# Kernel tuning notes

Hardware: AMD Instinct MI355X
Metric: run time of the kernel (lower is better)

Reference implementation:

```python
import jax, jax.numpy as jnp
import numpy as np

B, T, I, H, L, O = 512, 512, 64, 256, 3, 1  # batch, seq_len, input, hidden, layers, output


def setup_inputs() -> dict:
    key = jax.random.key(0)
    ks = jax.random.split(key, 16)
    s = 1.0 / np.sqrt(H)  # PyTorch nn.RNN init: U(-1/sqrt(H), 1/sqrt(H))
    u = lambda k, shape: jax.random.uniform(k, shape, jnp.float32, -s, s)
    inp = {"x": jax.random.normal(ks[0], (B, T, I), jnp.float32)}
    in_sizes = [I, H, H]
    for l in range(L):
        inp[f"w_ih{l}"] = u(ks[1 + 4 * l], (H, in_sizes[l]))
        inp[f"w_hh{l}"] = u(ks[2 + 4 * l], (H, H))
        inp[f"b_ih{l}"] = u(ks[3 + 4 * l], (H,))
        inp[f"b_hh{l}"] = u(ks[4 + 4 * l], (H,))
    inp["w_fc"] = u(ks[13], (O, H))
    inp["b_fc"] = u(ks[14], (O,))
    return inp


def _rnn_layer(x, w_ih, w_hh, b_ih, b_hh):
    # x: [B, T, in] -> outputs [B, T, H]; h_t = tanh(x_t W_ih^T + b_ih + h_{t-1} W_hh^T + b_hh)
    pre = jnp.einsum('bti,hi->bth', x, w_ih) + b_ih + b_hh  # input projection for all t at once

    def step(h, p_t):
        h = jnp.tanh(p_t + h @ w_hh.T)
        return h, h

    h0 = jnp.zeros((x.shape[0], w_hh.shape[0]), x.dtype)
    _, ys = jax.lax.scan(step, h0, pre.transpose(1, 0, 2))  # scan over time
    return ys.transpose(1, 0, 2)


def reference(x, w_ih0, w_hh0, b_ih0, b_hh0, w_ih1, w_hh1, b_ih1, b_hh1,
              w_ih2, w_hh2, b_ih2, b_hh2, w_fc, b_fc):
    h = _rnn_layer(x, w_ih0, w_hh0, b_ih0, b_hh0)
    h = _rnn_layer(h, w_ih1, w_hh1, b_ih1, b_hh1)
    h = _rnn_layer(h, w_ih2, w_hh2, b_ih2, b_hh2)
    out = h[:, -1, :] @ w_fc.T + b_fc  # [B, 1]
    return out.squeeze()  # [B]
```

## Files before the change

### kernel.cpp

```cpp
#include <hip/hip_runtime.h>
#include <cstdint>
#include <cstddef>

#define Tsz 512
#define TC  32
#define NCH 16

typedef _Float16 f16;
typedef _Float16 half8_t __attribute__((ext_vector_type(8)));
typedef _Float16 half4_t __attribute__((ext_vector_type(4)));
typedef float float4_t __attribute__((ext_vector_type(4)));

__device__ __forceinline__ float fast_exp2(float x) {
  float r; asm("v_exp_f32 %0, %1" : "=v"(r) : "v"(x)); return r;
}
__device__ __forceinline__ void pin(half8_t& v) { asm("" : "+v"(v)); }

#define BARRIER_LG asm volatile("s_waitcnt lgkmcnt(0)\n\ts_barrier" ::: "memory")

__device__ __forceinline__ size_t poff(int tile, int slot, int t, int j, int q) {
  return (((size_t)((tile * 2 + slot) * TC + t) * 256 + j) << 6) + ((size_t)q << 4);
}

template<int LAYER>
__device__ __forceinline__ void rec01_body(
    char* const smem, const int chunk, const int tile,
    const float* __restrict__ Pin, float* __restrict__ Pout,
    const f16* __restrict__ whh_h, const f16* __restrict__ wihn_h,
    const float* __restrict__ biasc, f16* __restrict__ st)
{
  char* const h_lds = smem;
  const int tid  = threadIdx.x;
  const int lane = tid & 63;
  const int wave = tid >> 6;
  const int m    = lane & 15;
  const int q    = lane >> 4;
  const int lo   = m * 16;
  const int slot = chunk & 1;

  half8_t whh[2][8], wihn[2][8];
  float biasn[2];
#pragma unroll
  for (int jt = 0; jt < 2; ++jt) {
    const int j = wave * 32 + jt * 16 + m;
    biasn[jt] = biasc[(LAYER + 1) * 256 + j];
#pragma unroll
    for (int c = 0; c < 8; ++c) whh[jt][c]  = *(const half8_t*)(whh_h  + j * 256 + c * 32 + q * 8);
#pragma unroll
    for (int c = 0; c < 8; ++c) wihn[jt][c] = *(const half8_t*)(wihn_h + j * 256 + c * 32 + q * 8);
  }
#pragma unroll
  for (int jt = 0; jt < 2; ++jt) {
#pragma unroll
    for (int c = 0; c < 8; ++c) { pin(whh[jt][c]); pin(wihn[jt][c]); }
  }

  if (chunk == 0)
    *(float4_t*)(h_lds + tid * 16) = float4_t{0.f, 0.f, 0.f, 0.f};
  else
    *(float4_t*)(h_lds + tid * 16) = *(const float4_t*)((const char*)st + tile * 8192 + tid * 16);

  float4_t pld[2][2];
  auto pload = [&](int tl, float4_t* d) {
    const int tn = (tl > TC - 1) ? (TC - 1) : tl;
    const char* gb = (const char*)Pin + poff(tile, slot, tn, wave * 32 + m, q);
    d[0] = *(const float4_t*)gb;
    d[1] = *(const float4_t*)(gb + 1024);
  };
  pload(0, pld[0]); pload(1, pld[1]);
  BARRIER_LG;

#pragma unroll 4
  for (int tl = 0; tl < TC; ++tl) {
    char* cur = h_lds + (tl & 1) * 8192;
    char* nxt = h_lds + ((tl + 1) & 1) * 8192;

    half8_t hf[8];
#pragma unroll
    for (int c = 0; c < 8; ++c) hf[c] = *(const half8_t*)(cur + (c * 4 + q) * 256 + lo);

    float4_t acc[2];
#pragma unroll
    for (int jt = 0; jt < 2; ++jt) {
      float4_t a = pld[tl & 1][jt];
#pragma unroll
      for (int c = 0; c < 8; ++c)
        a = __builtin_amdgcn_mfma_f32_16x16x32_f16(hf[c], whh[jt][c], a, 0, 0, 0);
      acc[jt] = a;
    }
    pload(tl + 2, pld[tl & 1]);

    if (tl >= 1) {
#pragma unroll
      for (int jt = 0; jt < 2; ++jt) {
        float4_t b = {biasn[jt], biasn[jt], biasn[jt], biasn[jt]};
#pragma unroll
        for (int c = 0; c < 8; ++c)
          b = __builtin_amdgcn_mfma_f32_16x16x32_f16(hf[c], wihn[jt][c], b, 0, 0, 0);
        *(float4_t*)((char*)Pout + poff(tile, slot, tl - 1, wave * 32 + jt * 16 + m, q)) = b;
      }
    }

#pragma unroll
    for (int jt = 0; jt < 2; ++jt) {
      const int j = wave * 32 + jt * 16 + m;
#pragma unroll
      for (int r = 0; r < 4; ++r) {
        const float e  = fast_exp2(acc[jt][r] * 2.8853900817779268f);
        const float hv = 1.0f - 2.0f * __builtin_amdgcn_rcpf(1.0f + e);
        const int b = q * 4 + r;
        *(f16*)(nxt + (j >> 3) * 256 + b * 16 + (j & 7) * 2) = (f16)hv;
      }
    }
    BARRIER_LG;
  }

  {
    half8_t hf[8];
#pragma unroll
    for (int c = 0; c < 8; ++c) hf[c] = *(const half8_t*)(h_lds + (c * 4 + q) * 256 + lo);
#pragma unroll
    for (int jt = 0; jt < 2; ++jt) {
      float4_t b = {biasn[jt], biasn[jt], biasn[jt], biasn[jt]};
#pragma unroll
      for (int c = 0; c < 8; ++c)
        b = __builtin_amdgcn_mfma_f32_16x16x32_f16(hf[c], wihn[jt][c], b, 0, 0, 0);
      *(float4_t*)((char*)Pout + poff(tile, slot, TC - 1, wave * 32 + jt * 16 + m, q)) = b;
    }
  }
  *(float4_t*)((char*)st + tile * 8192 + tid * 16) = *(const float4_t*)(h_lds + tid * 16);
}

template<bool REC, bool PRE>
__device__ __forceinline__ void l2_body(
    char* const smem, const int chunk, const int pre_chunk, const int tile,
    const float* __restrict__ x, const float* __restrict__ Pin, float* __restrict__ Pout,
    const f16* __restrict__ whh_h, const f16* __restrict__ wih0_h,
    const float* __restrict__ biasc, f16* __restrict__ st)
{
  char* const h_lds = smem;
  const int tid  = threadIdx.x;
  const int lane = tid & 63;
  const int wave = tid >> 6;
  const int m    = lane & 15;
  const int q    = lane >> 4;
  const int lo   = m * 16;
  const int slot  = chunk & 1;
  const int pslot = pre_chunk & 1;

  half8_t whh[2][8], wih0[2][2];
  float bias0[2];
#pragma unroll
  for (int jt = 0; jt < 2; ++jt) {
    const int j = wave * 32 + jt * 16 + m;
    if constexpr (PRE) {
      bias0[jt] = biasc[j];
#pragma unroll
      for (int c = 0; c < 2; ++c) wih0[jt][c] = *(const half8_t*)(wih0_h + j * 64 + c * 32 + q * 8);
    }
    if constexpr (REC) {
#pragma unroll
      for (int c = 0; c < 8; ++c) whh[jt][c] = *(const half8_t*)(whh_h + j * 256 + c * 32 + q * 8);
    }
  }
#pragma unroll
  for (int jt = 0; jt < 2; ++jt) {
    if constexpr (REC) {
#pragma unroll
      for (int c = 0; c < 8; ++c) pin(whh[jt][c]);
    }
    if constexpr (PRE) { pin(wih0[jt][0]); pin(wih0[jt][1]); }
  }

  float4_t pld[2][2];
  auto pload = [&](int tl, float4_t* d) {
    const int tn = (tl > TC - 1) ? (TC - 1) : tl;
    const char* gb = (const char*)Pin + poff(tile, slot, tn, wave * 32 + m, q);
    d[0] = *(const float4_t*)gb;
    d[1] = *(const float4_t*)(gb + 1024);
  };
  float4_t xp[2][4];
  auto xload = [&](int tl, float4_t* d) {
    const int tn = (tl > TC - 1) ? (TC - 1) : tl;
    const float* base = x + ((size_t)(tile * 16 + m) * Tsz + (pre_chunk * TC + tn)) * 64 + q * 8;
    d[0] = *(const float4_t*)base;        d[1] = *(const float4_t*)(base + 4);
    d[2] = *(const float4_t*)(base + 32); d[3] = *(const float4_t*)(base + 36);
  };

  if constexpr (REC) {
    if (chunk == 0)
      *(float4_t*)(h_lds + tid * 16) = float4_t{0.f, 0.f, 0.f, 0.f};
    else
      *(float4_t*)(h_lds + tid * 16) = *(const float4_t*)((const char*)st + tile * 8192 + tid * 16);
    pload(0, pld[0]); pload(1, pld[1]);
  }
  if constexpr (PRE) { xload(0, xp[0]); xload(1, xp[1]); }
  if constexpr (REC) BARRIER_LG;

#pragma unroll 4
  for (int tl = 0; tl < TC; ++tl) {
    if constexpr (REC) {
      char* cur = h_lds + (tl & 1) * 8192;
      char* nxt = h_lds + ((tl + 1) & 1) * 8192;
      half8_t hf[8];
#pragma unroll
      for (int c = 0; c < 8; ++c) hf[c] = *(const half8_t*)(cur + (c * 4 + q) * 256 + lo);
      float4_t acc[2];
#pragma unroll
      for (int jt = 0; jt < 2; ++jt) {
        float4_t a = pld[tl & 1][jt];
#pragma unroll
        for (int c = 0; c < 8; ++c)
          a = __builtin_amdgcn_mfma_f32_16x16x32_f16(hf[c], whh[jt][c], a, 0, 0, 0);
        acc[jt] = a;
      }
      pload(tl + 2, pld[tl & 1]);
#pragma unroll
      for (int jt = 0; jt < 2; ++jt) {
        const int j = wave * 32 + jt * 16 + m;
#pragma unroll
        for (int r = 0; r < 4; ++r) {
          const float e  = fast_exp2(acc[jt][r] * 2.8853900817779268f);
          const float hv = 1.0f - 2.0f * __builtin_amdgcn_rcpf(1.0f + e);
          const int b = q * 4 + r;
          *(f16*)(nxt + (j >> 3) * 256 + b * 16 + (j & 7) * 2) = (f16)hv;
        }
      }
    }
    if constexpr (PRE) {
      half8_t xf[2];
      const float4_t* xr = xp[tl & 1];
#pragma unroll
      for (int c = 0; c < 2; ++c)
#pragma unroll
        for (int u = 0; u < 8; ++u) xf[c][u] = (f16)xr[c * 2 + (u >> 2)][u & 3];
      xload(tl + 2, xp[tl & 1]);
#pragma unroll
      for (int jt = 0; jt < 2; ++jt) {
        float4_t b = {bias0[jt], bias0[jt], bias0[jt], bias0[jt]};
#pragma unroll
        for (int c = 0; c < 2; ++c)
          b = __builtin_amdgcn_mfma_f32_16x16x32_f16(xf[c], wih0[jt][c], b, 0, 0, 0);
        *(float4_t*)((char*)Pout + poff(tile, pslot, tl, wave * 32 + jt * 16 + m, q)) = b;
      }
    }
    if constexpr (REC) BARRIER_LG;
  }

  if constexpr (REC)
    *(float4_t*)((char*)st + tile * 8192 + tid * 16) = *(const float4_t*)(h_lds + tid * 16);
}

__global__ __launch_bounds__(512, 1)
void rnn_chunk_kernel(const float* __restrict__ x,
                      float* P0, float* P1, float* P2,
                      const f16* __restrict__ whh0h, const f16* __restrict__ whh1h,
                      const f16* __restrict__ whh2h, const f16* __restrict__ wih0h,
                      const f16* __restrict__ wih1h, const f16* __restrict__ wih2h,
                      const float* __restrict__ biasc,
                      f16* st0, f16* st1, f16* st2, int k)
{
  __shared__ __align__(16) char smem[16384];
  const int layer = blockIdx.x >> 5;
  const int tile  = blockIdx.x & 31;
  if (layer == 0) {
    if (k < NCH) rec01_body<0>(smem, k, tile, P0, P1, whh0h, wih1h, biasc, st0);
  } else if (layer == 1) {
    const int c = k - 1;
    if (c >= 0 && c < NCH) rec01_body<1>(smem, c, tile, P1, P2, whh1h, wih2h, biasc, st1);
  } else {
    const int c  = k - 2;
    const int pc = k + 1;
    const bool rec = (c >= 0 && c < NCH);
    const bool pre = (pc < NCH);
    if (rec && pre)  l2_body<true,  true >(smem, c, pc, tile, x, P2, P0, whh2h, wih0h, biasc, st2);
    else if (rec)    l2_body<true,  false>(smem, c, pc, tile, x, P2, P0, whh2h, wih0h, biasc, st2);
    else if (pre)    l2_body<false, true >(smem, c, pc, tile, x, P2, P0, whh2h, wih0h, biasc, st2);
  }
}

__global__ __launch_bounds__(512, 1)
void pre0_kernel(const float* __restrict__ x, float* P0,
                 const f16* __restrict__ wih0h, const float* __restrict__ biasc)
{
  __shared__ __align__(16) char smem[16384];
  l2_body<false, true>(smem, 0, 0, blockIdx.x, x, nullptr, P0, nullptr, wih0h, biasc, nullptr);
}

__global__ void prep_kernel(const float* __restrict__ wih0, const float* __restrict__ whh0,
                            const float* __restrict__ bih0, const float* __restrict__ bhh0,
                            const float* __restrict__ wih1, const float* __restrict__ whh1,
                            const float* __restrict__ bih1, const float* __restrict__ bhh1,
                            const float* __restrict__ wih2, const float* __restrict__ whh2,
                            const float* __restrict__ bih2, const float* __restrict__ bhh2,
                            f16* wih0h, f16* whh0h, f16* wih1h, f16* whh1h,
                            f16* wih2h, f16* whh2h, float* biasc)
{
  const int i = blockIdx.x * 256 + threadIdx.x;
  if      (i < 16384)  wih0h[i]          = (f16)wih0[i];
  else if (i < 81920)  whh0h[i - 16384]  = (f16)whh0[i - 16384];
  else if (i < 147456) wih1h[i - 81920]  = (f16)wih1[i - 81920];
  else if (i < 212992) whh1h[i - 147456] = (f16)whh1[i - 147456];
  else if (i < 278528) wih2h[i - 212992] = (f16)wih2[i - 212992];
  else if (i < 344064) whh2h[i - 278528] = (f16)whh2[i - 278528];
  else if (i < 344320) biasc[i - 344064]       = bih0[i - 344064] + bhh0[i - 344064];
  else if (i < 344576) biasc[256 + i - 344320] = bih1[i - 344320] + bhh1[i - 344320];
  else if (i < 344832) biasc[512 + i - 344576] = bih2[i - 344576] + bhh2[i - 344576];
}

__global__ void fc_kernel(const f16* __restrict__ st2, const float* __restrict__ w_fc,
                          const float* __restrict__ b_fc, float* __restrict__ outp) {
  const int b = blockIdx.x;
  const int lane = threadIdx.x;
  const int tile = b >> 4, bl = b & 15;
  const int j = lane * 4;
  const char* hp = (const char*)st2 + tile * 8192 + (j >> 3) * 256 + bl * 16 + (j & 7) * 2;
  const half4_t hv = *(const half4_t*)hp;
  const float4_t w = *(const float4_t*)(w_fc + j);
  float s = (float)hv[0] * w[0] + (float)hv[1] * w[1] + (float)hv[2] * w[2] + (float)hv[3] * w[3];
#pragma unroll
  for (int off = 32; off > 0; off >>= 1) s += __shfl_down(s, off, 64);
  if (lane == 0) outp[b] = s + b_fc[0];
}

extern "C" void kernel_launch(void* const* d_in, const int* in_sizes, int n_in,
                              void* d_out, int out_size, void* d_ws, size_t ws_size,
                              hipStream_t stream) {
  const float* x     = (const float*)d_in[0];
  const float* w_ih0 = (const float*)d_in[1];
  const float* w_hh0 = (const float*)d_in[2];
  const float* b_ih0 = (const float*)d_in[3];
  const float* b_hh0 = (const float*)d_in[4];
  const float* w_ih1 = (const float*)d_in[5];
  const float* w_hh1 = (const float*)d_in[6];
  const float* b_ih1 = (const float*)d_in[7];
  const float* b_hh1 = (const float*)d_in[8];
  const float* w_ih2 = (const float*)d_in[9];
  const float* w_hh2 = (const float*)d_in[10];
  const float* b_ih2 = (const float*)d_in[11];
  const float* b_hh2 = (const float*)d_in[12];
  const float* w_fc  = (const float*)d_in[13];
  const float* b_fc  = (const float*)d_in[14];

  char* ws = (char*)d_ws;
  float* P0   = (float*)(ws);
  float* P1   = (float*)(ws + 33554432);
  float* P2   = (float*)(ws + 67108864);
  f16* st0    = (f16*)(ws + 100663296);
  f16* st1    = (f16*)(ws + 100925440);
  f16* st2    = (f16*)(ws + 101187584);
  f16* wih0h  = (f16*)(ws + 101449728);
  f16* whh0h  = (f16*)(ws + 101482496);
  f16* wih1h  = (f16*)(ws + 101613568);
  f16* whh1h  = (f16*)(ws + 101744640);
  f16* wih2h  = (f16*)(ws + 101875712);
  f16* whh2h  = (f16*)(ws + 102006784);
  float* biasc = (float*)(ws + 102137856);

  prep_kernel<<<1347, 256, 0, stream>>>(w_ih0, w_hh0, b_ih0, b_hh0,
                                        w_ih1, w_hh1, b_ih1, b_hh1,
                                        w_ih2, w_hh2, b_ih2, b_hh2,
                                        wih0h, whh0h, wih1h, whh1h, wih2h, whh2h, biasc);
  pre0_kernel<<<32, 512, 0, stream>>>(x, P0, wih0h, biasc);
  for (int k = 0; k < NCH + 2; ++k)
    rnn_chunk_kernel<<<96, 512, 0, stream>>>(x, P0, P1, P2,
                                             whh0h, whh1h, whh2h,
                                             wih0h, wih1h, wih2h,
                                             biasc, st0, st1, st2, k);
  fc_kernel<<<512, 64, 0, stream>>>(st2, w_fc, b_fc, (float*)d_out);
}
```

Baseline: 1.033 ms.

## Halve waves per block, give each wave 64 hidden units, split MFMA accumulator chains

Each block now runs 4 waves of 256 threads instead of 8, so each wave owns 64 hidden columns (4 j-tiles) and holds twice as many weight registers. The MFMA reduction over K is split into two independent accumulator chains that are summed at the end, which shortens the serial dependency. The next-layer input projection is moved after the per-step barrier so it can overlap with other waves' work, and the barrier placement in the layer-2 body changes to match. Fewer waves means cheaper barriers but more register pressure and more serial MFMA work per wave on the recurrence critical path.

New measurement: 1.154 ms. 1.12x slower.

```diff
diff --git a/kernel.cpp b/kernel.cpp
--- a/kernel.cpp
+++ b/kernel.cpp
@@ -38,11 +38,11 @@
   const int lo   = m * 16;
   const int slot = chunk & 1;
 
-  half8_t whh[2][8], wihn[2][8];
-  float biasn[2];
-#pragma unroll
-  for (int jt = 0; jt < 2; ++jt) {
-    const int j = wave * 32 + jt * 16 + m;
+  half8_t whh[4][8], wihn[4][8];
+  float biasn[4];
+#pragma unroll
+  for (int jt = 0; jt < 4; ++jt) {
+    const int j = wave * 64 + jt * 16 + m;
     biasn[jt] = biasc[(LAYER + 1) * 256 + j];
 #pragma unroll
     for (int c = 0; c < 8; ++c) whh[jt][c]  = *(const half8_t*)(whh_h  + j * 256 + c * 32 + q * 8);
@@ -50,27 +50,30 @@
     for (int c = 0; c < 8; ++c) wihn[jt][c] = *(const half8_t*)(wihn_h + j * 256 + c * 32 + q * 8);
   }
 #pragma unroll
-  for (int jt = 0; jt < 2; ++jt) {
+  for (int jt = 0; jt < 4; ++jt) {
 #pragma unroll
     for (int c = 0; c < 8; ++c) { pin(whh[jt][c]); pin(wihn[jt][c]); }
   }
 
-  if (chunk == 0)
-    *(float4_t*)(h_lds + tid * 16) = float4_t{0.f, 0.f, 0.f, 0.f};
-  else
-    *(float4_t*)(h_lds + tid * 16) = *(const float4_t*)((const char*)st + tile * 8192 + tid * 16);
-
-  float4_t pld[2][2];
+  if (chunk == 0) {
+    *(float4_t*)(h_lds + tid * 32)      = float4_t{0.f, 0.f, 0.f, 0.f};
+    *(float4_t*)(h_lds + tid * 32 + 16) = float4_t{0.f, 0.f, 0.f, 0.f};
+  } else {
+    *(float4_t*)(h_lds + tid * 32)      = *(const float4_t*)((const char*)st + tile * 8192 + tid * 32);
+    *(float4_t*)(h_lds + tid * 32 + 16) = *(const float4_t*)((const char*)st + tile * 8192 + tid * 32 + 16);
+  }
+
+  float4_t pld[2][4];
   auto pload = [&](int tl, float4_t* d) {
     const int tn = (tl > TC - 1) ? (TC - 1) : tl;
-    const char* gb = (const char*)Pin + poff(tile, slot, tn, wave * 32 + m, q);
-    d[0] = *(const float4_t*)gb;
-    d[1] = *(const float4_t*)(gb + 1024);
+    const char* gb = (const char*)Pin + poff(tile, slot, tn, wave * 64 + m, q);
+#pragma unroll
+    for (int jt = 0; jt < 4; ++jt) d[jt] = *(const float4_t*)(gb + jt * 1024);
   };
   pload(0, pld[0]); pload(1, pld[1]);
   BARRIER_LG;
 
-#pragma unroll 4
+#pragma unroll 2
   for (int tl = 0; tl < TC; ++tl) {
     char* cur = h_lds + (tl & 1) * 8192;
     char* nxt = h_lds + ((tl + 1) & 1) * 8192;
@@ -79,31 +82,23 @@
 #pragma unroll
     for (int c = 0; c < 8; ++c) hf[c] = *(const half8_t*)(cur + (c * 4 + q) * 256 + lo);
 
-    float4_t acc[2];
-#pragma unroll
-    for (int jt = 0; jt < 2; ++jt) {
-      float4_t a = pld[tl & 1][jt];
-#pragma unroll
-      for (int c = 0; c < 8; ++c)
-        a = __builtin_amdgcn_mfma_f32_16x16x32_f16(hf[c], whh[jt][c], a, 0, 0, 0);
-      acc[jt] = a;
+    float4_t acc[4];
+#pragma unroll
+    for (int jt = 0; jt < 4; ++jt) {
+      float4_t a0 = pld[tl & 1][jt];
+      float4_t a1 = {0.f, 0.f, 0.f, 0.f};
+#pragma unroll
+      for (int c = 0; c < 4; ++c) {
+        a0 = __builtin_amdgcn_mfma_f32_16x16x32_f16(hf[c],     whh[jt][c],     a0, 0, 0, 0);
+        a1 = __builtin_amdgcn_mfma_f32_16x16x32_f16(hf[c + 4], whh[jt][c + 4], a1, 0, 0, 0);
+      }
+      acc[jt] = a0 + a1;
     }
     pload(tl + 2, pld[tl & 1]);
 
-    if (tl >= 1) {
-#pragma unroll
-      for (int jt = 0; jt < 2; ++jt) {
-        float4_t b = {biasn[jt], biasn[jt], biasn[jt], biasn[jt]};
-#pragma unroll
-        for (int c = 0; c < 8; ++c)
-          b = __builtin_amdgcn_mfma_f32_16x16x32_f16(hf[c], wihn[jt][c], b, 0, 0, 0);
-        *(float4_t*)((char*)Pout + poff(tile, slot, tl - 1, wave * 32 + jt * 16 + m, q)) = b;
-      }
-    }
-
-#pragma unroll
-    for (int jt = 0; jt < 2; ++jt) {
-      const int j = wave * 32 + jt * 16 + m;
+#pragma unroll
+    for (int jt = 0; jt < 4; ++jt) {
+      const int j = wave * 64 + jt * 16 + m;
 #pragma unroll
       for (int r = 0; r < 4; ++r) {
         const float e  = fast_exp2(acc[jt][r] * 2.8853900817779268f);
@@ -113,6 +108,21 @@
       }
     }
     BARRIER_LG;
+
+    if (tl >= 1) {
+#pragma unroll
+      for (int jt = 0; jt < 4; ++jt) {
+        float4_t b0 = {biasn[jt], biasn[jt], biasn[jt], biasn[jt]};
+        float4_t b1 = {0.f, 0.f, 0.f, 0.f};
+#pragma unroll
+        for (int c = 0; c < 4; ++c) {
+          b0 = __builtin_amdgcn_mfma_f32_16x16x32_f16(hf[c],     wihn[jt][c],     b0, 0, 0, 0);
+          b1 = __builtin_amdgcn_mfma_f32_16x16x32_f16(hf[c + 4], wihn[jt][c + 4], b1, 0, 0, 0);
+        }
+        float4_t b = b0 + b1;
+        *(float4_t*)((char*)Pout + poff(tile, slot, tl - 1, wave * 64 + jt * 16 + m, q)) = b;
+      }
+    }
   }
 
   {
@@ -120,15 +130,20 @@
 #pragma unroll
     for (int c = 0; c < 8; ++c) hf[c] = *(const half8_t*)(h_lds + (c * 4 + q) * 256 + lo);
 #pragma unroll
-    for (int jt = 0; jt < 2; ++jt) {
-      float4_t b = {biasn[jt], biasn[jt], biasn[jt], biasn[jt]};
-#pragma unroll
-      for (int c = 0; c < 8; ++c)
-        b = __builtin_amdgcn_mfma_f32_16x16x32_f16(hf[c], wihn[jt][c], b, 0, 0, 0);
-      *(float4_t*)((char*)Pout + poff(tile, slot, TC - 1, wave * 32 + jt * 16 + m, q)) = b;
-    }
-  }
-  *(float4_t*)((char*)st + tile * 8192 + tid * 16) = *(const float4_t*)(h_lds + tid * 16);
+    for (int jt = 0; jt < 4; ++jt) {
+      float4_t b0 = {biasn[jt], biasn[jt], biasn[jt], biasn[jt]};
+      float4_t b1 = {0.f, 0.f, 0.f, 0.f};
+#pragma unroll
+      for (int c = 0; c < 4; ++c) {
+        b0 = __builtin_amdgcn_mfma_f32_16x16x32_f16(hf[c],     wihn[jt][c],     b0, 0, 0, 0);
+        b1 = __builtin_amdgcn_mfma_f32_16x16x32_f16(hf[c + 4], wihn[jt][c + 4], b1, 0, 0, 0);
+      }
+      float4_t b = b0 + b1;
+      *(float4_t*)((char*)Pout + poff(tile, slot, TC - 1, wave * 64 + jt * 16 + m, q)) = b;
+    }
+  }
+  *(float4_t*)((char*)st + tile * 8192 + tid * 32)      = *(const float4_t*)(h_lds + tid * 32);
+  *(float4_t*)((char*)st + tile * 8192 + tid * 32 + 16) = *(const float4_t*)(h_lds + tid * 32 + 16);
 }
 
 template<bool REC, bool PRE>
@@ -148,11 +163,11 @@
   const int slot  = chunk & 1;
   const int pslot = pre_chunk & 1;
 
-  half8_t whh[2][8], wih0[2][2];
-  float bias0[2];
-#pragma unroll
-  for (int jt = 0; jt < 2; ++jt) {
-    const int j = wave * 32 + jt * 16 + m;
+  half8_t whh[4][8], wih0[4][2];
+  float bias0[4];
+#pragma unroll
+  for (int jt = 0; jt < 4; ++jt) {
+    const int j = wave * 64 + jt * 16 + m;
     if constexpr (PRE) {
       bias0[jt] = biasc[j];
 #pragma unroll
@@ -164,7 +179,7 @@
     }
   }
 #pragma unroll
-  for (int jt = 0; jt < 2; ++jt) {
+  for (int jt = 0; jt < 4; ++jt) {
     if constexpr (REC) {
 #pragma unroll
       for (int c = 0; c < 8; ++c) pin(whh[jt][c]);
@@ -172,12 +187,12 @@
     if constexpr (PRE) { pin(wih0[jt][0]); pin(wih0[jt][1]); }
   }
 
-  float4_t pld[2][2];
+  float4_t pld[2][4];
   auto pload = [&](int tl, float4_t* d) {
     const int tn = (tl > TC - 1) ? (TC - 1) : tl;
-    const char* gb = (const char*)Pin + poff(tile, slot, tn, wave * 32 + m, q);
-    d[0] = *(const float4_t*)gb;
-    d[1] = *(const float4_t*)(gb + 1024);
+    const char* gb = (const char*)Pin + poff(tile, slot, tn, wave * 64 + m, q);
+#pragma unroll
+    for (int jt = 0; jt < 4; ++jt) d[jt] = *(const float4_t*)(gb + jt * 1024);
   };
   float4_t xp[2][4];
   auto xload = [&](int tl, float4_t* d) {
@@ -188,16 +203,19 @@
   };
 
   if constexpr (REC) {
-    if (chunk == 0)
-      *(float4_t*)(h_lds + tid * 16) = float4_t{0.f, 0.f, 0.f, 0.f};
-    else
-      *(float4_t*)(h_lds + tid * 16) = *(const float4_t*)((const char*)st + tile * 8192 + tid * 16);
+    if (chunk == 0) {
+      *(float4_t*)(h_lds + tid * 32)      = float4_t{0.f, 0.f, 0.f, 0.f};
+      *(float4_t*)(h_lds + tid * 32 + 16) = float4_t{0.f, 0.f, 0.f, 0.f};
+    } else {
+      *(float4_t*)(h_lds + tid * 32)      = *(const float4_t*)((const char*)st + tile * 8192 + tid * 32);
+      *(float4_t*)(h_lds + tid * 32 + 16) = *(const float4_t*)((const char*)st + tile * 8192 + tid * 32 + 16);
+    }
     pload(0, pld[0]); pload(1, pld[1]);
   }
   if constexpr (PRE) { xload(0, xp[0]); xload(1, xp[1]); }
   if constexpr (REC) BARRIER_LG;
 
-#pragma unroll 4
+#pragma unroll 2
   for (int tl = 0; tl < TC; ++tl) {
     if constexpr (REC) {
       char* cur = h_lds + (tl & 1) * 8192;
@@ -205,19 +223,22 @@
       half8_t hf[8];
 #pragma unroll
       for (int c = 0; c < 8; ++c) hf[c] = *(const half8_t*)(cur + (c * 4 + q) * 256 + lo);
-      float4_t acc[2];
-#pragma unroll
-      for (int jt = 0; jt < 2; ++jt) {
-        float4_t a = pld[tl & 1][jt];
-#pragma unroll
-        for (int c = 0; c < 8; ++c)
-          a = __builtin_amdgcn_mfma_f32_16x16x32_f16(hf[c], whh[jt][c], a, 0, 0, 0);
-        acc[jt] = a;
+      float4_t acc[4];
+#pragma unroll
+      for (int jt = 0; jt < 4; ++jt) {
+        float4_t a0 = pld[tl & 1][jt];
+        float4_t a1 = {0.f, 0.f, 0.f, 0.f};
+#pragma unroll
+        for (int c = 0; c < 4; ++c) {
+          a0 = __builtin_amdgcn_mfma_f32_16x16x32_f16(hf[c],     whh[jt][c],     a0, 0, 0, 0);
+          a1 = __builtin_amdgcn_mfma_f32_16x16x32_f16(hf[c + 4], whh[jt][c + 4], a1, 0, 0, 0);
+        }
+        acc[jt] = a0 + a1;
       }
       pload(tl + 2, pld[tl & 1]);
 #pragma unroll
-      for (int jt = 0; jt < 2; ++jt) {
-        const int j = wave * 32 + jt * 16 + m;
+      for (int jt = 0; jt < 4; ++jt) {
+        const int j = wave * 64 + jt * 16 + m;
 #pragma unroll
         for (int r = 0; r < 4; ++r) {
           const float e  = fast_exp2(acc[jt][r] * 2.8853900817779268f);
@@ -227,6 +248,7 @@
         }
       }
     }
+    if constexpr (REC) BARRIER_LG;
     if constexpr (PRE) {
       half8_t xf[2];
       const float4_t* xr = xp[tl & 1];
@@ -236,22 +258,23 @@
         for (int u = 0; u < 8; ++u) xf[c][u] = (f16)xr[c * 2 + (u >> 2)][u & 3];
       xload(tl + 2, xp[tl & 1]);
 #pragma unroll
-      for (int jt = 0; jt < 2; ++jt) {
+      for (int jt = 0; jt < 4; ++jt) {
         float4_t b = {bias0[jt], bias0[jt], bias0[jt], bias0[jt]};
 #pragma unroll
         for (int c = 0; c < 2; ++c)
           b = __builtin_amdgcn_mfma_f32_16x16x32_f16(xf[c], wih0[jt][c], b, 0, 0, 0);
-        *(float4_t*)((char*)Pout + poff(tile, pslot, tl, wave * 32 + jt * 16 + m, q)) = b;
-      }
-    }
-    if constexpr (REC) BARRIER_LG;
-  }
-
-  if constexpr (REC)
-    *(float4_t*)((char*)st + tile * 8192 + tid * 16) = *(const float4_t*)(h_lds + tid * 16);
-}
-
-__global__ __launch_bounds__(512, 1)
+        *(float4_t*)((char*)Pout + poff(tile, pslot, tl, wave * 64 + jt * 16 + m, q)) = b;
+      }
+    }
+  }
+
+  if constexpr (REC) {
+    *(float4_t*)((char*)st + tile * 8192 + tid * 32)      = *(const float4_t*)(h_lds + tid * 32);
+    *(float4_t*)((char*)st + tile * 8192 + tid * 32 + 16) = *(const float4_t*)(h_lds + tid * 32 + 16);
+  }
+}
+
+__global__ __launch_bounds__(256, 1)
 void rnn_chunk_kernel(const float* __restrict__ x,
                       float* P0, float* P1, float* P2,
                       const f16* __restrict__ whh0h, const f16* __restrict__ whh1h,
@@ -279,7 +302,7 @@
   }
 }
 
-__global__ __launch_bounds__(512, 1)
+__global__ __launch_bounds__(256, 1)
 void pre0_kernel(const float* __restrict__ x, float* P0,
                  const f16* __restrict__ wih0h, const float* __restrict__ biasc)
 {
@@ -361,9 +384,9 @@
                                         w_ih1, w_hh1, b_ih1, b_hh1,
                                         w_ih2, w_hh2, b_ih2, b_hh2,
                                         wih0h, whh0h, wih1h, whh1h, wih2h, whh2h, biasc);
-  pre0_kernel<<<32, 512, 0, stream>>>(x, P0, wih0h, biasc);
+  pre0_kernel<<<32, 256, 0, stream>>>(x, P0, wih0h, biasc);
   for (int k = 0; k < NCH + 2; ++k)
-    rnn_chunk_kernel<<<96, 512, 0, stream>>>(x, P0, P1, P2,
+    rnn_chunk_kernel<<<96, 256, 0, stream>>>(x, P0, P1, P2,
                                              whh0h, whh1h, whh2h,
                                              wih0h, wih1h, wih2h,
                                              biasc, st0, st1, st2, k);
```

## Double waves per block so each wave owns one 16-column hidden tile

Applied to the files above, without the earlier changes.

Blocks grow from 512 to 1024 threads, so each wave handles a single 16-column slice of the hidden state instead of two. This halves the per-wave MFMA chain length on the serial recurrence and halves weight register pressure. The K loop is split into two half accumulators that are summed afterward. The input x is also converted to fp16 once in a new prep kernel, which removes per-step float-to-half conversion in the layer-0 projection. The cost is more waves contending at each barrier, a larger barrier, and an extra pass over x.

After: 954.0 us. 7.7% less time.

```diff
diff --git a/kernel.cpp b/kernel.cpp
--- a/kernel.cpp
+++ b/kernel.cpp
@@ -37,104 +37,98 @@
   const int q    = lane >> 4;
   const int lo   = m * 16;
   const int slot = chunk & 1;
-
-  half8_t whh[2][8], wihn[2][8];
-  float biasn[2];
-#pragma unroll
-  for (int jt = 0; jt < 2; ++jt) {
-    const int j = wave * 32 + jt * 16 + m;
-    biasn[jt] = biasc[(LAYER + 1) * 256 + j];
-#pragma unroll
-    for (int c = 0; c < 8; ++c) whh[jt][c]  = *(const half8_t*)(whh_h  + j * 256 + c * 32 + q * 8);
-#pragma unroll
-    for (int c = 0; c < 8; ++c) wihn[jt][c] = *(const half8_t*)(wihn_h + j * 256 + c * 32 + q * 8);
-  }
-#pragma unroll
-  for (int jt = 0; jt < 2; ++jt) {
-#pragma unroll
-    for (int c = 0; c < 8; ++c) { pin(whh[jt][c]); pin(wihn[jt][c]); }
-  }
-
-  if (chunk == 0)
-    *(float4_t*)(h_lds + tid * 16) = float4_t{0.f, 0.f, 0.f, 0.f};
-  else
-    *(float4_t*)(h_lds + tid * 16) = *(const float4_t*)((const char*)st + tile * 8192 + tid * 16);
-
-  float4_t pld[2][2];
+  const int j    = wave * 16 + m;
+
+  half8_t whh[8], wihn[8];
+  float biasn = biasc[(LAYER + 1) * 256 + j];
+#pragma unroll
+  for (int c = 0; c < 8; ++c) whh[c]  = *(const half8_t*)(whh_h  + j * 256 + c * 32 + q * 8);
+#pragma unroll
+  for (int c = 0; c < 8; ++c) wihn[c] = *(const half8_t*)(wihn_h + j * 256 + c * 32 + q * 8);
+#pragma unroll
+  for (int c = 0; c < 8; ++c) { pin(whh[c]); pin(wihn[c]); }
+
+  if (tid < 512) {
+    if (chunk == 0)
+      *(float4_t*)(h_lds + tid * 16) = float4_t{0.f, 0.f, 0.f, 0.f};
+    else
+      *(float4_t*)(h_lds + tid * 16) = *(const float4_t*)((const char*)st + tile * 8192 + tid * 16);
+  }
+
+  float4_t pld[2];
   auto pload = [&](int tl, float4_t* d) {
     const int tn = (tl > TC - 1) ? (TC - 1) : tl;
-    const char* gb = (const char*)Pin + poff(tile, slot, tn, wave * 32 + m, q);
-    d[0] = *(const float4_t*)gb;
-    d[1] = *(const float4_t*)(gb + 1024);
+    d[0] = *(const float4_t*)((const char*)Pin + poff(tile, slot, tn, j, q));
   };
-  pload(0, pld[0]); pload(1, pld[1]);
+  pload(0, &pld[0]); pload(1, &pld[1]);
   BARRIER_LG;
 
-#pragma unroll 4
+#pragma unroll 2
   for (int tl = 0; tl < TC; ++tl) {
     char* cur = h_lds + (tl & 1) * 8192;
     char* nxt = h_lds + ((tl + 1) & 1) * 8192;
 
-    half8_t hf[8];
-#pragma unroll
-    for (int c = 0; c < 8; ++c) hf[c] = *(const half8_t*)(cur + (c * 4 + q) * 256 + lo);
-
-    float4_t acc[2];
-#pragma unroll
-    for (int jt = 0; jt < 2; ++jt) {
-      float4_t a = pld[tl & 1][jt];
-#pragma unroll
-      for (int c = 0; c < 8; ++c)
-        a = __builtin_amdgcn_mfma_f32_16x16x32_f16(hf[c], whh[jt][c], a, 0, 0, 0);
-      acc[jt] = a;
-    }
-    pload(tl + 2, pld[tl & 1]);
-
+    half8_t hf[4];
+#pragma unroll
+    for (int c = 0; c < 4; ++c) hf[c] = *(const half8_t*)(cur + (c * 4 + q) * 256 + lo);
+    float4_t a0 = pld[tl & 1];
+#pragma unroll
+    for (int c = 0; c < 4; ++c)
+      a0 = __builtin_amdgcn_mfma_f32_16x16x32_f16(hf[c], whh[c], a0, 0, 0, 0);
+    float4_t b0 = {biasn, biasn, biasn, biasn};
     if (tl >= 1) {
 #pragma unroll
-      for (int jt = 0; jt < 2; ++jt) {
-        float4_t b = {biasn[jt], biasn[jt], biasn[jt], biasn[jt]};
-#pragma unroll
-        for (int c = 0; c < 8; ++c)
-          b = __builtin_amdgcn_mfma_f32_16x16x32_f16(hf[c], wihn[jt][c], b, 0, 0, 0);
-        *(float4_t*)((char*)Pout + poff(tile, slot, tl - 1, wave * 32 + jt * 16 + m, q)) = b;
-      }
-    }
-
-#pragma unroll
-    for (int jt = 0; jt < 2; ++jt) {
-      const int j = wave * 32 + jt * 16 + m;
-#pragma unroll
-      for (int r = 0; r < 4; ++r) {
-        const float e  = fast_exp2(acc[jt][r] * 2.8853900817779268f);
-        const float hv = 1.0f - 2.0f * __builtin_amdgcn_rcpf(1.0f + e);
-        const int b = q * 4 + r;
-        *(f16*)(nxt + (j >> 3) * 256 + b * 16 + (j & 7) * 2) = (f16)hv;
-      }
+      for (int c = 0; c < 4; ++c)
+        b0 = __builtin_amdgcn_mfma_f32_16x16x32_f16(hf[c], wihn[c], b0, 0, 0, 0);
+    }
+#pragma unroll
+    for (int c = 0; c < 4; ++c) hf[c] = *(const half8_t*)(cur + ((c + 4) * 4 + q) * 256 + lo);
+    float4_t a1 = {0.f, 0.f, 0.f, 0.f};
+#pragma unroll
+    for (int c = 0; c < 4; ++c)
+      a1 = __builtin_amdgcn_mfma_f32_16x16x32_f16(hf[c], whh[c + 4], a1, 0, 0, 0);
+    if (tl >= 1) {
+#pragma unroll
+      for (int c = 0; c < 4; ++c)
+        b0 = __builtin_amdgcn_mfma_f32_16x16x32_f16(hf[c], wihn[c + 4], b0, 0, 0, 0);
+      *(float4_t*)((char*)Pout + poff(tile, slot, tl - 1, j, q)) = b0;
+    }
+    pload(tl + 2, &pld[tl & 1]);
+
+    const float4_t acc = a0 + a1;
+#pragma unroll
+    for (int r = 0; r < 4; ++r) {
+      const float e  = fast_exp2(acc[r] * 2.8853900817779268f);
+      const float hv = 1.0f - 2.0f * __builtin_amdgcn_rcpf(1.0f + e);
+      const int b = q * 4 + r;
+      *(f16*)(nxt + (j >> 3) * 256 + b * 16 + (j & 7) * 2) = (f16)hv;
     }
     BARRIER_LG;
   }
 
   {
-    half8_t hf[8];
-#pragma unroll
-    for (int c = 0; c < 8; ++c) hf[c] = *(const half8_t*)(h_lds + (c * 4 + q) * 256 + lo);
-#pragma unroll
-    for (int jt = 0; jt < 2; ++jt) {
-      float4_t b = {biasn[jt], biasn[jt], biasn[jt], biasn[jt]};
-#pragma unroll
-      for (int c = 0; c < 8; ++c)
-        b = __builtin_amdgcn_mfma_f32_16x16x32_f16(hf[c], wihn[jt][c], b, 0, 0, 0);
-      *(float4_t*)((char*)Pout + poff(tile, slot, TC - 1, wave * 32 + jt * 16 + m, q)) = b;
-    }
-  }
-  *(float4_t*)((char*)st + tile * 8192 + tid * 16) = *(const float4_t*)(h_lds + tid * 16);
+    half8_t hf[4];
+    float4_t b0 = {biasn, biasn, biasn, biasn};
+#pragma unroll
+    for (int c = 0; c < 4; ++c) hf[c] = *(const half8_t*)(h_lds + (c * 4 + q) * 256 + lo);
+#pragma unroll
+    for (int c = 0; c < 4; ++c)
+      b0 = __builtin_amdgcn_mfma_f32_16x16x32_f16(hf[c], wihn[c], b0, 0, 0, 0);
+#pragma unroll
+    for (int c = 0; c < 4; ++c) hf[c] = *(const half8_t*)(h_lds + ((c + 4) * 4 + q) * 256 + lo);
+#pragma unroll
+    for (int c = 0; c < 4; ++c)
+      b0 = __builtin_amdgcn_mfma_f32_16x16x32_f16(hf[c], wihn[c + 4], b0, 0, 0, 0);
+    *(float4_t*)((char*)Pout + poff(tile, slot, TC - 1, j, q)) = b0;
+  }
+  if (tid < 512)
+    *(float4_t*)((char*)st + tile * 8192 + tid * 16) = *(const float4_t*)(h_lds + tid * 16);
 }
 
 template<bool REC, bool PRE>
 __device__ __forceinline__ void l2_body(
     char* const smem, const int chunk, const int pre_chunk, const int tile,
-    const float* __restrict__ x, const float* __restrict__ Pin, float* __restrict__ Pout,
+    const f16* __restrict__ xh, const float* __restrict__ Pin, float* __restrict__ Pout,
     const f16* __restrict__ whh_h, const f16* __restrict__ wih0_h,
     const float* __restrict__ biasc, f16* __restrict__ st)
 {
@@ -147,112 +141,94 @@
   const int lo   = m * 16;
   const int slot  = chunk & 1;
   const int pslot = pre_chunk & 1;
-
-  half8_t whh[2][8], wih0[2][2];
-  float bias0[2];
-#pragma unroll
-  for (int jt = 0; jt < 2; ++jt) {
-    const int j = wave * 32 + jt * 16 + m;
-    if constexpr (PRE) {
-      bias0[jt] = biasc[j];
-#pragma unroll
-      for (int c = 0; c < 2; ++c) wih0[jt][c] = *(const half8_t*)(wih0_h + j * 64 + c * 32 + q * 8);
-    }
-    if constexpr (REC) {
-#pragma unroll
-      for (int c = 0; c < 8; ++c) whh[jt][c] = *(const half8_t*)(whh_h + j * 256 + c * 32 + q * 8);
-    }
-  }
-#pragma unroll
-  for (int jt = 0; jt < 2; ++jt) {
-    if constexpr (REC) {
-#pragma unroll
-      for (int c = 0; c < 8; ++c) pin(whh[jt][c]);
-    }
-    if constexpr (PRE) { pin(wih0[jt][0]); pin(wih0[jt][1]); }
-  }
-
-  float4_t pld[2][2];
+  const int j    = wave * 16 + m;
+
+  half8_t whh[8], wih0[2];
+  float bias0 = 0.f;
+  if constexpr (PRE) {
+    bias0 = biasc[j];
+#pragma unroll
+    for (int c = 0; c < 2; ++c) wih0[c] = *(const half8_t*)(wih0_h + j * 64 + c * 32 + q * 8);
+    pin(wih0[0]); pin(wih0[1]);
+  }
+  if constexpr (REC) {
+#pragma unroll
+    for (int c = 0; c < 8; ++c) whh[c] = *(const half8_t*)(whh_h + j * 256 + c * 32 + q * 8);
+#pragma unroll
+    for (int c = 0; c < 8; ++c) pin(whh[c]);
+  }
+
+  float4_t pld[2];
   auto pload = [&](int tl, float4_t* d) {
     const int tn = (tl > TC - 1) ? (TC - 1) : tl;
-    const char* gb = (const char*)Pin + poff(tile, slot, tn, wave * 32 + m, q);
-    d[0] = *(const float4_t*)gb;
-    d[1] = *(const float4_t*)(gb + 1024);
+    d[0] = *(const float4_t*)((const char*)Pin + poff(tile, slot, tn, j, q));
   };
-  float4_t xp[2][4];
-  auto xload = [&](int tl, float4_t* d) {
+  half8_t xp[2][2];
+  auto xload = [&](int tl, half8_t* d) {
     const int tn = (tl > TC - 1) ? (TC - 1) : tl;
-    const float* base = x + ((size_t)(tile * 16 + m) * Tsz + (pre_chunk * TC + tn)) * 64 + q * 8;
-    d[0] = *(const float4_t*)base;        d[1] = *(const float4_t*)(base + 4);
-    d[2] = *(const float4_t*)(base + 32); d[3] = *(const float4_t*)(base + 36);
+    const f16* base = xh + ((size_t)(tile * 16 + m) * Tsz + (pre_chunk * TC + tn)) * 64 + q * 8;
+    d[0] = *(const half8_t*)base;
+    d[1] = *(const half8_t*)(base + 32);
   };
 
   if constexpr (REC) {
-    if (chunk == 0)
-      *(float4_t*)(h_lds + tid * 16) = float4_t{0.f, 0.f, 0.f, 0.f};
-    else
-      *(float4_t*)(h_lds + tid * 16) = *(const float4_t*)((const char*)st + tile * 8192 + tid * 16);
-    pload(0, pld[0]); pload(1, pld[1]);
+    if (tid < 512) {
+      if (chunk == 0)
+        *(float4_t*)(h_lds + tid * 16) = float4_t{0.f, 0.f, 0.f, 0.f};
+      else
+        *(float4_t*)(h_lds + tid * 16) = *(const float4_t*)((const char*)st + tile * 8192 + tid * 16);
+    }
+    pload(0, &pld[0]); pload(1, &pld[1]);
   }
   if constexpr (PRE) { xload(0, xp[0]); xload(1, xp[1]); }
   if constexpr (REC) BARRIER_LG;
 
-#pragma unroll 4
+#pragma unroll 2
   for (int tl = 0; tl < TC; ++tl) {
     if constexpr (REC) {
       char* cur = h_lds + (tl & 1) * 8192;
       char* nxt = h_lds + ((tl + 1) & 1) * 8192;
-      half8_t hf[8];
-#pragma unroll
-      for (int c = 0; c < 8; ++c) hf[c] = *(const half8_t*)(cur + (c * 4 + q) * 256 + lo);
-      float4_t acc[2];
-#pragma unroll
-      for (int jt = 0; jt < 2; ++jt) {
-        float4_t a = pld[tl & 1][jt];
-#pragma unroll
-        for (int c = 0; c < 8; ++c)
-          a = __builtin_amdgcn_mfma_f32_16x16x32_f16(hf[c], whh[jt][c], a, 0, 0, 0);
-        acc[jt] = a;
+      half8_t hf[4];
+#pragma unroll
+      for (int c = 0; c < 4; ++c) hf[c] = *(const half8_t*)(cur + (c * 4 + q) * 256 + lo);
+      float4_t a0 = pld[tl & 1];
+#pragma unroll
+      for (int c = 0; c < 4; ++c)
+        a0 = __builtin_amdgcn_mfma_f32_16x16x32_f16(hf[c], whh[c], a0, 0, 0, 0);
+#pragma unroll
+      for (int c = 0; c < 4; ++c) hf[c] = *(const half8_t*)(cur + ((c + 4) * 4 + q) * 256 + lo);
+      float4_t a1 = {0.f, 0.f, 0.f, 0.f};
+#pragma unroll
+      for (int c = 0; c < 4; ++c)
+        a1 = __builtin_amdgcn_mfma_f32_16x16x32_f16(hf[c], whh[c + 4], a1, 0, 0, 0);
+      pload(tl + 2, &pld[tl & 1]);
+      const float4_t acc = a0 + a1;
+#pragma unroll
+      for (int r = 0; r < 4; ++r) {
+        const float e  = fast_exp2(acc[r] * 2.8853900817779268f);
+        const float hv = 1.0f - 2.0f * __builtin_amdgcn_rcpf(1.0f + e);
+        const int b = q * 4 + r;
+        *(f16*)(nxt + (j >> 3) * 256 + b * 16 + (j & 7) * 2) = (f16)hv;
       }
-      pload(tl + 2, pld[tl & 1]);
-#pragma unroll
-      for (int jt = 0; jt < 2; ++jt) {
-        const int j = wave * 32 + jt * 16 + m;
-#pragma unroll
-        for (int r = 0; r < 4; ++r) {
-          const float e  = fast_exp2(acc[jt][r] * 2.8853900817779268f);
-          const float hv = 1.0f - 2.0f * __builtin_amdgcn_rcpf(1.0f + e);
-          const int b = q * 4 + r;
-          *(f16*)(nxt + (j >> 3) * 256 + b * 16 + (j & 7) * 2) = (f16)hv;
-        }
-      }
     }
     if constexpr (PRE) {
-      half8_t xf[2];
-      const float4_t* xr = xp[tl & 1];
-#pragma unroll
-      for (int c = 0; c < 2; ++c)
-#pragma unroll
-        for (int u = 0; u < 8; ++u) xf[c][u] = (f16)xr[c * 2 + (u >> 2)][u & 3];
+      float4_t b = {bias0, bias0, bias0, bias0};
+      b = __builtin_amdgcn_mfma_f32_16x16x32_f16(xp[tl & 1][0], wih0[0], b, 0, 0, 0);
+      b = __builtin_amdgcn_mfma_f32_16x16x32_f16(xp[tl & 1][1], wih0[1], b, 0, 0, 0);
       xload(tl + 2, xp[tl & 1]);
-#pragma unroll
-      for (int jt = 0; jt < 2; ++jt) {
-        float4_t b = {bias0[jt], bias0[jt], bias0[jt], bias0[jt]};
-#pragma unroll
-        for (int c = 0; c < 2; ++c)
-          b = __builtin_amdgcn_mfma_f32_16x16x32_f16(xf[c], wih0[jt][c], b, 0, 0, 0);
-        *(float4_t*)((char*)Pout + poff(tile, pslot, tl, wave * 32 + jt * 16 + m, q)) = b;
-      }
+      *(float4_t*)((char*)Pout + poff(tile, pslot, tl, j, q)) = b;
     }
     if constexpr (REC) BARRIER_LG;
   }
 
-  if constexpr (REC)
-    *(float4_t*)((char*)st + tile * 8192 + tid * 16) = *(const float4_t*)(h_lds + tid * 16);
-}
-
-__global__ __launch_bounds__(512, 1)
-void rnn_chunk_kernel(const float* __restrict__ x,
+  if constexpr (REC) {
+    if (tid < 512)
+      *(float4_t*)((char*)st + tile * 8192 + tid * 16) = *(const float4_t*)(h_lds + tid * 16);
+  }
+}
+
+__global__ __launch_bounds__(1024)
+void rnn_chunk_kernel(const f16* __restrict__ xh,
                       float* P0, float* P1, float* P2,
                       const f16* __restrict__ whh0h, const f16* __restrict__ whh1h,
                       const f16* __restrict__ whh2h, const f16* __restrict__ wih0h,
@@ -273,18 +249,28 @@
     const int pc = k + 1;
     const bool rec = (c >= 0 && c < NCH);
     const bool pre = (pc < NCH);
-    if (rec && pre)  l2_body<true,  true >(smem, c, pc, tile, x, P2, P0, whh2h, wih0h, biasc, st2);
-    else if (rec)    l2_body<true,  false>(smem, c, pc, tile, x, P2, P0, whh2h, wih0h, biasc, st2);
-    else if (pre)    l2_body<false, true >(smem, c, pc, tile, x, P2, P0, whh2h, wih0h, biasc, st2);
-  }
-}
-
-__global__ __launch_bounds__(512, 1)
-void pre0_kernel(const float* __restrict__ x, float* P0,
+    if (rec && pre)  l2_body<true,  true >(smem, c, pc, tile, xh, P2, P0, whh2h, wih0h, biasc, st2);
+    else if (rec)    l2_body<true,  false>(smem, c, pc, tile, xh, P2, P0, whh2h, wih0h, biasc, st2);
+    else if (pre)    l2_body<false, true >(smem, c, pc, tile, xh, P2, P0, whh2h, wih0h, biasc, st2);
+  }
+}
+
+__global__ __launch_bounds__(1024)
+void pre0_kernel(const f16* __restrict__ xh, float* P0,
                  const f16* __restrict__ wih0h, const float* __restrict__ biasc)
 {
   __shared__ __align__(16) char smem[16384];
-  l2_body<false, true>(smem, 0, 0, blockIdx.x, x, nullptr, P0, nullptr, wih0h, biasc, nullptr);
+  l2_body<false, true>(smem, 0, 0, blockIdx.x, xh, nullptr, P0, nullptr, wih0h, biasc, nullptr);
+}
+
+__global__ void prep_x_kernel(const float* __restrict__ x, f16* __restrict__ xh) {
+  const size_t i = ((size_t)blockIdx.x * 256 + threadIdx.x) * 8;
+  const float4_t v0 = *(const float4_t*)(x + i);
+  const float4_t v1 = *(const float4_t*)(x + i + 4);
+  half8_t o;
+#pragma unroll
+  for (int u = 0; u < 4; ++u) { o[u] = (f16)v0[u]; o[u + 4] = (f16)v1[u]; }
+  *(half8_t*)(xh + i) = o;
 }
 
 __global__ void prep_kernel(const float* __restrict__ wih0, const float* __restrict__ whh0,
@@ -356,16 +342,18 @@
   f16* wih2h  = (f16*)(ws + 101875712);
   f16* whh2h  = (f16*)(ws + 102006784);
   float* biasc = (float*)(ws + 102137856);
-
+  f16* xh     = (f16*)(ws + 102141952);
+
+  prep_x_kernel<<<8192, 256, 0, stream>>>(x, xh);
   prep_kernel<<<1347, 256, 0, stream>>>(w_ih0, w_hh0, b_ih0, b_hh0,
                                         w_ih1, w_hh1, b_ih1, b_hh1,
                                         w_ih2, w_hh2, b_ih2, b_hh2,
                                         wih0h, whh0h, wih1h, whh1h, wih2h, whh2h, biasc);
-  pre0_kernel<<<32, 512, 0, stream>>>(x, P0, wih0h, biasc);
+  pre0_kernel<<<32, 1024, 0, stream>>>(xh, P0, wih0h, biasc);
   for (int k = 0; k < NCH + 2; ++k)
-    rnn_chunk_kernel<<<96, 512, 0, stream>>>(x, P0, P1, P2,
-                                             whh0h, whh1h, whh2h,
-                                             wih0h, wih1h, wih2h,
-                                             biasc, st0, st1, st2, k);
+    rnn_chunk_kernel<<<96, 1024, 0, stream>>>(xh, P0, P1, P2,
+                                              whh0h, whh1h, whh2h,
+                                              wih0h, wih1h, wih2h,
+                                              biasc, st0, st1, st2, k);
   fc_kernel<<<512, 64, 0, stream>>>(st2, w_fc, b_fc, (float*)d_out);
 }
```
